# Optimization experiments

Measured on AMD Instinct MI355X. Metric: run time of the kernel, lower is better.

## Reference

```python
import jax, jax.numpy as jnp
import numpy as np

B, DIM, HEADS = 8, 1024, 8
DH = DIM // HEADS            # 128 = dim_head
MFEAT = 621                  # int(DH * log(DH)) performer features
MAXD = 4                     # max_rel_dist
IMG = 10                     # image side; source hardcodes stride 10 in scatter indices
L = IMG * IMG + 1            # geometry forces L = img_dim**2 + 1


def _geometry():
    m, K = MAXD, 2 * MAXD - 1
    base = np.arange(-m + 1, m)
    dx = np.broadcast_to(np.tile(base, K), (L, K * K))
    dy = np.broadcast_to(np.repeat(base, K), (L, K * K))
    x_off = np.concatenate([np.tile(np.arange(IMG), IMG), [0]])[:, None]
    y_off = np.concatenate([np.repeat(np.arange(IMG), IMG), [IMG]])[:, None]
    x_pos, y_pos = dx + x_off, dy + y_off
    diffs = np.abs(dx) + np.abs(dy)
    valid = (x_pos >= 0) & (x_pos < IMG) & (y_pos >= 0) & (y_pos < IMG) & (diffs < m)
    diffs = np.where(valid, diffs, m)  # invalid taps point at the max-dist encoding
    rel_window = (m - 1) * IMG + (m - 1)
    # scatter positions inside the unfold window (stride 10 hardcoded in source)
    indices = np.tile(np.arange(K), K) + np.repeat(np.arange(K) * 10, K)
    return jnp.asarray(diffs), jnp.asarray(valid), jnp.asarray(indices - rel_window)

DIFFS, VALID, OFFSETS = _geometry()  # [L,K2] int, [L,K2] bool, [K2] int


def softmax_kernel(data, proj, is_query, eps=1e-4):
    dn = data.shape[-1] ** -0.25
    ratio = proj.shape[0] ** -0.5
    dd = jnp.einsum('...id,jd->...ij', data * dn, proj)
    diag = (jnp.sum(data ** 2, -1) * (0.5 * dn * dn))[..., None]
    mx = jnp.max(dd, -1, keepdims=True) if is_query else jnp.max(dd)
    return ratio * (jnp.exp(dd - diag - mx) + eps)


def relative_attention(q, rpe, v):
    # q: [b,h,L,MFEAT] kernel features, rpe: [R,MFEAT], v: [b,h,L,DH]
    mde = rpe[-1]                                   # max-distance encoding
    v_sum = v.sum(-2)                               # [b,h,DH]
    q_dot = jnp.einsum('bhlm,rm->bhlr', q, rpe - mde)
    q_rel = jnp.take_along_axis(q_dot, DIFFS[None, None], axis=-1)  # [b,h,L,K2]
    q_rel = jnp.where(VALID[None, None], q_rel, 0.0)
    # gather v at relative offsets (equivalent to the zero-padded unfold +
    # sparse scatter of q_rel in the source, without the dense 67-wide window)
    pos = jnp.arange(L)[:, None] + OFFSETS[None, :]  # [L,K2]
    inb = (pos >= 0) & (pos < L)
    v_g = v[:, :, jnp.clip(pos, 0, L - 1), :]        # [b,h,L,K2,DH]
    v_g = jnp.where(inb[None, None, :, :, None], v_g, 0.0)
    denom = (rpe[DIFFS] - mde).sum(1) + mde * L      # [L,MFEAT]
    D_inv = 1.0 / jnp.einsum('bhlm,lm->bhl', q, denom)
    q_md = jnp.einsum('bhlm,m->bhl', q, mde)
    out = jnp.einsum('bhl,bhd->bhld', q_md, v_sum) + jnp.einsum('bhlk,bhlkd->bhld', q_rel, v_g)
    return out * D_inv[..., None]


def setup_inputs() -> dict:
    key = jax.random.key(0)
    ks = jax.random.split(key, 9)
    s = DIM ** -0.5
    return {
        'x': jax.random.normal(ks[0], (B, L, DIM), jnp.float32),
        'Wq': jax.random.normal(ks[1], (DIM, DIM), jnp.float32) * s,
        'bq': jnp.zeros((DIM,), jnp.float32),
        'Wv': jax.random.normal(ks[2], (DIM, DIM), jnp.float32) * s,
        'bv': jnp.zeros((DIM,), jnp.float32),
        'rpe': jax.random.normal(ks[3], (MAXD + 1, DH), jnp.float32) * 0.02,
        'proj': jax.random.normal(ks[4], (MFEAT, DH), jnp.float32),
        'Wo': jax.random.normal(ks[5], (DIM, DIM), jnp.float32) * s,
        'bo': jnp.zeros((DIM,), jnp.float32),
    }


def reference(x, Wq, bq, Wv, bv, rpe, proj, Wo, bo):
    b = x.shape[0]
    q = (x @ Wq.T + bq).reshape(b, L, HEADS, DH).transpose(0, 2, 1, 3)
    v = (x @ Wv.T + bv).reshape(b, L, HEADS, DH).transpose(0, 2, 1, 3)
    qf = softmax_kernel(q, proj, is_query=True)
    rf = softmax_kernel(rpe[None, None], proj, is_query=False)[0, 0]
    out = relative_attention(qf, rf, v)          # [b,h,L,DH]
    out = out.transpose(0, 2, 1, 3).reshape(b, L, DIM)
    return out @ Wo.T + bo
```

## Files before the change

kernel.cpp:

```cpp
#include <hip/hip_runtime.h>
#include <math.h>

namespace {

typedef __bf16 bf16_t;
typedef bf16_t bf16x8 __attribute__((ext_vector_type(8)));
typedef bf16_t bf16x4 __attribute__((ext_vector_type(4)));
typedef float f32x4 __attribute__((ext_vector_type(4)));

constexpr int B = 8, L = 101, DIM = 1024, H = 8, DH = 128, MF = 621, MFP = 640;
constexpr int BL = B * L;
constexpr int BLP = 832;
constexpr int BH = B * H;
constexpr int RR = BL * H;

constexpr float DN    = 0.29730177875068026f;
constexpr float DN2   = 0.08838834764831845f;
constexpr float RATIO = 0.04012861672f;
constexpr float EPS   = 1e-4f;

constexpr int NX = BL * DIM / 4;
constexpr int NP = MFP * 32;
constexpr int NR = 64 * DH / 4;
constexpr int NW = DIM * DIM / 4;
constexpr int NZ = 4 * (BLP - BL) * DIM / 4;
constexpr int NTOT = NX + NP + NR + 3 * NW + NZ;

__device__ __forceinline__ f32x4 mfma16(bf16x8 a, bf16x8 b, f32x4 c) {
  return __builtin_amdgcn_mfma_f32_16x16x32_bf16(a, b, c, 0, 0, 0);
}

__device__ __forceinline__ void split2(float f, bf16_t& h, bf16_t& l) {
  h = (bf16_t)f;
  l = (bf16_t)(f - (float)h);
}

__device__ __forceinline__ void gload_lds16(const bf16_t* g, bf16_t* l) {
  __builtin_amdgcn_global_load_lds(
      (const __attribute__((address_space(1))) void*)g,
      (__attribute__((address_space(3))) void*)l, 16, 0, 0);
}

__global__ __launch_bounds__(256) void split_all(const float* __restrict__ x,
                                                 const float* __restrict__ proj,
                                                 const float* __restrict__ rpe,
                                                 const float* __restrict__ Wq,
                                                 const float* __restrict__ Wv,
                                                 const float* __restrict__ Wo,
                                                 bf16_t* __restrict__ xh, bf16_t* __restrict__ xl,
                                                 bf16_t* __restrict__ ph,
                                                 bf16_t* __restrict__ rh, bf16_t* __restrict__ rl,
                                                 bf16_t* __restrict__ Wh,
                                                 bf16_t* __restrict__ Woh,
                                                 bf16_t* __restrict__ qh, bf16_t* __restrict__ ql) {
  const int u = blockIdx.x * 256 + threadIdx.x;
  if (u >= NTOT) return;
  auto emit2 = [](const float* s4, float sc, bf16_t* dh, bf16_t* dl, size_t off) {
    float4 f = *(const float4*)s4;
    bf16x4 hv, lv; bf16_t h, l;
    split2(f.x * sc, h, l); hv[0] = h; lv[0] = l;
    split2(f.y * sc, h, l); hv[1] = h; lv[1] = l;
    split2(f.z * sc, h, l); hv[2] = h; lv[2] = l;
    split2(f.w * sc, h, l); hv[3] = h; lv[3] = l;
    *(bf16x4*)(dh + off) = hv;
    *(bf16x4*)(dl + off) = lv;
  };
  auto emit1 = [](const float* s4, float sc, bf16_t* dh, size_t off) {
    float4 f = *(const float4*)s4;
    bf16x4 hv;
    hv[0] = (bf16_t)(f.x * sc); hv[1] = (bf16_t)(f.y * sc);
    hv[2] = (bf16_t)(f.z * sc); hv[3] = (bf16_t)(f.w * sc);
    *(bf16x4*)(dh + off) = hv;
  };
  int t = u;
  if (t < NX) { emit2(x + (size_t)t * 4, 1.f, xh, xl, (size_t)t * 4); return; }
  t -= NX;
  if (t < NP) {
    if ((t >> 5) < MF) emit1(proj + (size_t)t * 4, DN, ph, (size_t)t * 4);
    else { bf16x4 z = {}; *(bf16x4*)(ph + (size_t)t * 4) = z; }
    return;
  }
  t -= NP;
  if (t < NR) {
    if (t < 5 * DH / 4) emit2(rpe + (size_t)t * 4, 1.f, rh, rl, (size_t)t * 4);
    else { bf16x4 z = {}; *(bf16x4*)(rh + (size_t)t * 4) = z; *(bf16x4*)(rl + (size_t)t * 4) = z; }
    return;
  }
  t -= NR;
  if (t < NW) { emit1(Wq + (size_t)t * 4, 1.f, Wh, (size_t)t * 4); return; }
  t -= NW;
  if (t < NW) { emit1(Wv + (size_t)t * 4, 1.f, Wh, (size_t)(t + NW) * 4); return; }
  t -= NW;
  if (t < NW) { emit1(Wo + (size_t)t * 4, 1.f, Woh, (size_t)t * 4); return; }
  t -= NW;
  {
    const int buf = t / 6144, o = t % 6144;
    bf16_t* dst = (buf == 0) ? xh : (buf == 1) ? xl : (buf == 2) ? qh : ql;
    bf16x4 z = {};
    *(bf16x4*)(dst + (size_t)BL * DIM + (size_t)o * 4) = z;
  }
}

template<int MODE>
__global__ __launch_bounds__(256) void gemm64(const bf16_t* __restrict__ Ah,
                                              const bf16_t* __restrict__ Al,
                                              const bf16_t* __restrict__ Bh,
                                              const float* __restrict__ bias0,
                                              const float* __restrict__ bias1,
                                              float* __restrict__ Cf,
                                              bf16_t* __restrict__ Ch,
                                              bf16_t* __restrict__ Cl) {
  constexpr int K = 1024, BK = 64, NK = K / BK;
  __shared__ bf16_t lds[2][3][64 * 64];
  const int tid = threadIdx.x;
  const int w = tid >> 6, lane = tid & 63;
  const int wr = w >> 1, wc = w & 1;
  const int l15 = lane & 15, l4 = lane >> 4;
  const int rowBase = blockIdx.y * 64, colBase = blockIdx.x * 64;
  const int r8 = lane >> 3;
  const int cs = (lane & 7) ^ r8;
  const bf16_t* src = (w == 0) ? Ah : (w == 1) ? Al : Bh;
  const int grow0 = (w < 2) ? rowBase : colBase + ((w == 3) ? 32 : 0);
  const bf16_t* srcL = src + (size_t)(grow0 + r8) * K + cs * 8;
  const int tt = (w < 2) ? w : 2;
  const int dst0 = (w == 3) ? 32 * 64 : 0;
  auto STAGE = [&](int bf, int k0) {
    if (w < 2) {
#pragma unroll
      for (int j = 0; j < 8; ++j)
        gload_lds16(srcL + (size_t)(8 * j) * K + k0, &lds[bf][tt][j * 512]);
    } else {
#pragma unroll
      for (int j = 0; j < 4; ++j)
        gload_lds16(srcL + (size_t)(8 * j) * K + k0, &lds[bf][2][dst0 + j * 512]);
    }
  };
  const int ra0 = wr * 32 + l15, ra1 = ra0 + 16;
  const int rb0 = wc * 32 + l15, rb1 = rb0 + 16;
  auto TADDR = [](int row, int kg) { return row * 64 + (((kg) ^ (row & 7)) << 3); };
  f32x4 acc[2][2] = {};
  STAGE(0, 0);
  __syncthreads();
  int bf = 0;
  for (int ks = 0; ks < NK; ++ks) {
    if (ks + 1 < NK) STAGE(bf ^ 1, (ks + 1) * BK);
#pragma unroll
    for (int subk = 0; subk < 2; ++subk) {
      const int kg = subk * 4 + l4;
      bf16x8 a0h = *(const bf16x8*)&lds[bf][0][TADDR(ra0, kg)];
      bf16x8 a0l = *(const bf16x8*)&lds[bf][1][TADDR(ra0, kg)];
      bf16x8 a1h = *(const bf16x8*)&lds[bf][0][TADDR(ra1, kg)];
      bf16x8 a1l = *(const bf16x8*)&lds[bf][1][TADDR(ra1, kg)];
      bf16x8 b0  = *(const bf16x8*)&lds[bf][2][TADDR(rb0, kg)];
      bf16x8 b1  = *(const bf16x8*)&lds[bf][2][TADDR(rb1, kg)];
      acc[0][0] = mfma16(a0h, b0, acc[0][0]);
      acc[0][0] = mfma16(a0l, b0, acc[0][0]);
      acc[0][1] = mfma16(a0h, b1, acc[0][1]);
      acc[0][1] = mfma16(a0l, b1, acc[0][1]);
      acc[1][0] = mfma16(a1h, b0, acc[1][0]);
      acc[1][0] = mfma16(a1l, b0, acc[1][0]);
      acc[1][1] = mfma16(a1h, b1, acc[1][1]);
      acc[1][1] = mfma16(a1l, b1, acc[1][1]);
    }
    __syncthreads();
    bf ^= 1;
  }
#pragma unroll
  for (int ni = 0; ni < 2; ++ni) {
    const int col = colBase + wc * 32 + ni * 16 + l15;
#pragma unroll
    for (int mi = 0; mi < 2; ++mi) {
#pragma unroll
      for (int r2 = 0; r2 < 4; ++r2) {
        const int row = rowBase + wr * 32 + mi * 16 + l4 * 4 + r2;
        if (row < BL) {
          if (MODE == 0) {
            Cf[(size_t)row * 1024 + col] = acc[mi][ni][r2] + bias0[col];
          } else {
            if (col < 1024) {
              float val = acc[mi][ni][r2] + bias0[col];
              bf16_t h, lo; split2(val, h, lo);
              Ch[(size_t)row * 1024 + col] = h;
              Cl[(size_t)row * 1024 + col] = lo;
            } else {
              Cf[(size_t)row * 1024 + (col - 1024)] = acc[mi][ni][r2] + bias1[col - 1024];
            }
          }
        }
      }
    }
  }
}

__global__ __launch_bounds__(256) void qf3_kernel(const bf16_t* __restrict__ qh,
                                                  const bf16_t* __restrict__ ql,
                                                  const bf16_t* __restrict__ rh,
                                                  const bf16_t* __restrict__ rl,
                                                  const bf16_t* __restrict__ ph,
                                                  const float* __restrict__ rpe,
                                                  const float* __restrict__ v,
                                                  float* __restrict__ vsum,
                                                  float* __restrict__ fd) {
  const int tid = threadIdx.x;
  if (blockIdx.x >= 202) {
    const int bi = blockIdx.x - 202;
    const int half = tid >> 7, d = tid & 127;
    const int bh = bi * 2 + half;
    const int b = bh >> 3, h = bh & 7;
    const float* base = v + (size_t)(b * L) * DIM + h * DH + d;
    float s0 = 0.f, s1 = 0.f, s2 = 0.f, s3 = 0.f;
    int l = 0;
    for (; l + 4 <= L; l += 4) {
      s0 += base[(size_t)l * DIM];
      s1 += base[(size_t)(l + 1) * DIM];
      s2 += base[(size_t)(l + 2) * DIM];
      s3 += base[(size_t)(l + 3) * DIM];
    }
    for (; l < L; ++l) s0 += base[(size_t)l * DIM];
    vsum[(size_t)bh * DH + d] = s0 + s1 + s2 + s3;
    return;
  }
  __shared__ bf16_t Ahl[2][64 * 128];
  __shared__ bf16_t Bch[2][64 * 128];
  __shared__ float rfs[5][MFP];
  __shared__ float diag[32];
  __shared__ float diag5v[8];
  __shared__ float mxs[4][32];
  __shared__ float mxAll[32];
  __shared__ float mxrf[4];
  __shared__ float sred[4][32][5];
  const int w = tid >> 6, lane = tid & 63;
  const int l15 = lane & 15, l4 = lane >> 4;
  const int r0 = blockIdx.x * 32;
  const int r4 = lane >> 4;
  const int cg = lane & 15;
  {
    const bf16_t* srcA = (w == 0) ? qh : (w == 1) ? ql : (w == 2) ? rh : rl;
    const int arow0 = (w < 2) ? r0 : 0;
    bf16_t* dstA = &Ahl[w & 1][(w >= 2 ? 32 : 0) * 128];
    const bf16_t* peA = srcA + (size_t)(arow0 + r4) * DH + ((cg ^ r4) << 3);
    const bf16_t* poA = srcA + (size_t)(arow0 + r4) * DH + ((cg ^ r4 ^ 4) << 3);
#pragma unroll
    for (int j = 0; j < 8; ++j)
      gload_lds16(((j & 1) ? poA : peA) + (size_t)(4 * j) * DH, dstA + j * 512);
  }
  const bf16_t* peB = ph + (size_t)(w * 16 + r4) * DH + ((cg ^ r4) << 3);
  const bf16_t* poB = ph + (size_t)(w * 16 + r4) * DH + ((cg ^ r4 ^ 4) << 3);
  auto STAGE_B = [&](int buf, int c) {
    const size_t coff = (size_t)c * 64 * DH;
#pragma unroll
    for (int j = 0; j < 4; ++j)
      gload_lds16(((j & 1) ? poB : peB) + coff + (size_t)(4 * j) * DH,
                  &Bch[buf][(w * 16 + j * 4) * 128]);
  };
  {
    const int row = tid >> 3, ch = tid & 7;
    const size_t base = (size_t)(r0 + row) * DH + ch * 16;
    float s = 0.f;
#pragma unroll
    for (int t = 0; t < 2; ++t) {
      bf16x8 vh = *(const bf16x8*)(qh + base + t * 8);
      bf16x8 vl = *(const bf16x8*)(ql + base + t * 8);
#pragma unroll
      for (int e = 0; e < 8; ++e) {
        float f = (float)vh[e] + (float)vl[e];
        s += f * f;
      }
    }
    s += __shfl_xor(s, 1, 64); s += __shfl_xor(s, 2, 64); s += __shfl_xor(s, 4, 64);
    if (ch == 0) diag[row] = (0.5f * DN2) * s;
  }
  if (tid < 40) {
    const int row = tid >> 3, ch = tid & 7;
    float s = 0.f;
#pragma unroll
    for (int e = 0; e < 16; ++e) { float f = rpe[row * DH + ch * 16 + e]; s += f * f; }
    s += __shfl_xor(s, 1, 64); s += __shfl_xor(s, 2, 64); s += __shfl_xor(s, 4, 64);
    if (ch == 0) diag5v[row] = (0.5f * DN2) * s;
  }
  auto TADDR = [](int row, int kg) { return row * 128 + (((kg) ^ (row & 7)) << 3); };
  f32x4 acc[2][10] = {};
  f32x4 accr[10] = {};
  STAGE_B(0, 0);
  __syncthreads();
  int buf = 0;
#pragma unroll
  for (int c = 0; c < 10; ++c) {
    if (c + 1 < 10) STAGE_B(buf ^ 1, c + 1);
#pragma unroll
    for (int ks = 0; ks < 4; ++ks) {
      const int kg = ks * 4 + l4;
      bf16x8 a0h = *(const bf16x8*)&Ahl[0][TADDR(l15, kg)];
      bf16x8 a0l = *(const bf16x8*)&Ahl[1][TADDR(l15, kg)];
      bf16x8 a1h = *(const bf16x8*)&Ahl[0][TADDR(16 + l15, kg)];
      bf16x8 a1l = *(const bf16x8*)&Ahl[1][TADDR(16 + l15, kg)];
      bf16x8 arh = *(const bf16x8*)&Ahl[0][TADDR(32 + l15, kg)];
      bf16x8 arl = *(const bf16x8*)&Ahl[1][TADDR(32 + l15, kg)];
      bf16x8 bb  = *(const bf16x8*)&Bch[buf][TADDR(w * 16 + l15, kg)];
      acc[0][c] = mfma16(a0h, bb, acc[0][c]);
      acc[0][c] = mfma16(a0l, bb, acc[0][c]);
      acc[1][c] = mfma16(a1h, bb, acc[1][c]);
      acc[1][c] = mfma16(a1l, bb, acc[1][c]);
      accr[c]   = mfma16(arh, bb, accr[c]);
      accr[c]   = mfma16(arl, bb, accr[c]);
    }
    __syncthreads();
    buf ^= 1;
  }
  float pm[2][4];
#pragma unroll
  for (int mi = 0; mi < 2; ++mi)
#pragma unroll
    for (int r2 = 0; r2 < 4; ++r2) {
      float m = -3.4e38f;
#pragma unroll
      for (int ni = 0; ni < 10; ++ni) {
        const int col = ni * 64 + w * 16 + l15;
        float vv = (col < MF) ? acc[mi][ni][r2] : -3.4e38f;
        m = fmaxf(m, vv);
      }
      pm[mi][r2] = m;
    }
#pragma unroll
  for (int mask = 1; mask <= 8; mask <<= 1)
#pragma unroll
    for (int mi = 0; mi < 2; ++mi)
#pragma unroll
      for (int r2 = 0; r2 < 4; ++r2)
        pm[mi][r2] = fmaxf(pm[mi][r2], __shfl_xor(pm[mi][r2], mask, 64));
  if (l15 == 0) {
#pragma unroll
    for (int mi = 0; mi < 2; ++mi)
#pragma unroll
      for (int r2 = 0; r2 < 4; ++r2)
        mxs[w][mi * 16 + l4 * 4 + r2] = pm[mi][r2];
  }
  {
    float m = -3.4e38f;
#pragma unroll
    for (int ni = 0; ni < 10; ++ni) {
      const int col = ni * 64 + w * 16 + l15;
#pragma unroll
      for (int r2 = 0; r2 < 4; ++r2) {
        const int row5 = l4 * 4 + r2;
        if (row5 < 5 && col < MF) m = fmaxf(m, accr[ni][r2]);
      }
    }
#pragma unroll
    for (int mask = 1; mask <= 32; mask <<= 1) m = fmaxf(m, __shfl_xor(m, mask, 64));
    if (lane == 0) mxrf[w] = m;
  }
  __syncthreads();
  {
    const float mxR = fmaxf(fmaxf(mxrf[0], mxrf[1]), fmaxf(mxrf[2], mxrf[3]));
#pragma unroll
    for (int ni = 0; ni < 10; ++ni) {
      const int col = ni * 64 + w * 16 + l15;
#pragma unroll
      for (int r2 = 0; r2 < 4; ++r2) {
        const int row5 = l4 * 4 + r2;
        if (row5 < 5) {
          float val = (col < MF)
              ? RATIO * (__expf(accr[ni][r2] - diag5v[row5] - mxR) + EPS) : 0.f;
          rfs[row5][col] = val;
        }
      }
    }
  }
  if (tid < 32)
    mxAll[tid] = fmaxf(fmaxf(mxs[0][tid], mxs[1][tid]), fmaxf(mxs[2][tid], mxs[3][tid]));
  __syncthreads();
  for (int i = tid; i < 4 * MFP; i += 256) rfs[i / MFP][i % MFP] -= rfs[4][i % MFP];
  __syncthreads();
  float s[2][4][5] = {};
#pragma unroll
  for (int mi = 0; mi < 2; ++mi)
#pragma unroll
    for (int r2 = 0; r2 < 4; ++r2) {
      const int row = mi * 16 + l4 * 4 + r2;
      const float sub = diag[row] + mxAll[row];
#pragma unroll
      for (int ni = 0; ni < 10; ++ni) {
        const int col = ni * 64 + w * 16 + l15;
        const float qfv = RATIO * (__expf(acc[mi][ni][r2] - sub) + EPS);
#pragma unroll
        for (int c = 0; c < 5; ++c) s[mi][r2][c] += qfv * rfs[c][col];
      }
    }
#pragma unroll
  for (int mask = 1; mask <= 8; mask <<= 1)
#pragma unroll
    for (int mi = 0; mi < 2; ++mi)
#pragma unroll
      for (int r2 = 0; r2 < 4; ++r2)
#pragma unroll
        for (int c = 0; c < 5; ++c)
          s[mi][r2][c] += __shfl_xor(s[mi][r2][c], mask, 64);
  if (l15 == 0) {
#pragma unroll
    for (int mi = 0; mi < 2; ++mi)
#pragma unroll
      for (int r2 = 0; r2 < 4; ++r2)
#pragma unroll
        for (int c = 0; c < 5; ++c)
          sred[w][mi * 16 + l4 * 4 + r2][c] = s[mi][r2][c];
  }
  __syncthreads();
  if (tid < 160) {
    const int row = tid / 5, c = tid % 5;
    fd[(size_t)(r0 + row) * 8 + c] =
        sred[0][row][c] + sred[1][row][c] + sred[2][row][c] + sred[3][row][c];
  }
}

__global__ __launch_bounds__(256) void out_kernel(const float* __restrict__ fd,
                                                  const float* __restrict__ v,
                                                  const float* __restrict__ vsum,
                                                  bf16_t* __restrict__ attnh,
                                                  bf16_t* __restrict__ attnl) {
  const int tid = threadIdx.x;
  const int sub = tid >> 7, d = tid & 127;
  const int bh = blockIdx.y, b = bh >> 3, h = bh & 7;
  const int l = blockIdx.x * 2 + sub;
  if (l >= L) return;
  const size_t r = (size_t)(b * L + l) * H + h;
  const float q0 = fd[r * 8 + 0], q1 = fd[r * 8 + 1], q2 = fd[r * 8 + 2],
              q3 = fd[r * 8 + 3], sM = fd[r * 8 + 4];
  float o = sM * vsum[(size_t)bh * DH + d];
  float c0 = 0, c1 = 0, c2 = 0, c3 = 0;
  const int xo = (l < 100) ? (l % 10) : 0;
  const int yo = (l < 100) ? (l / 10) : 10;
#pragma unroll
  for (int k = 0; k < 49; ++k) {
    const int dx = (k % 7) - 3, dy = (k / 7) - 3;
    const int xp = xo + dx, yp = yo + dy;
    const int df = (dx < 0 ? -dx : dx) + (dy < 0 ? -dy : dy);
    if (xp >= 0 && xp < 10 && yp >= 0 && yp < 10 && df < 4) {
      float qq;
      if (df == 0)      { c0 += 1.f; qq = q0; }
      else if (df == 1) { c1 += 1.f; qq = q1; }
      else if (df == 2) { c2 += 1.f; qq = q2; }
      else              { c3 += 1.f; qq = q3; }
      const int pos = l + dx + 10 * dy;
      o += qq * v[(size_t)(b * L + pos) * DIM + h * DH + d];
    }
  }
  const float D = c0 * q0 + c1 * q1 + c2 * q2 + c3 * q3 + (float)L * sM;
  const float val = o / D;
  bf16_t hi, lo; split2(val, hi, lo);
  const size_t oi = (size_t)(b * L + l) * DIM + h * DH + d;
  attnh[oi] = hi;
  attnl[oi] = lo;
}

}

extern "C" void kernel_launch(void* const* d_in, const int* in_sizes, int n_in,
                              void* d_out, int out_size, void* d_ws, size_t ws_size,
                              hipStream_t stream) {
  const float* x    = (const float*)d_in[0];
  const float* Wq   = (const float*)d_in[1];
  const float* bq   = (const float*)d_in[2];
  const float* Wv   = (const float*)d_in[3];
  const float* bv   = (const float*)d_in[4];
  const float* rpe  = (const float*)d_in[5];
  const float* proj = (const float*)d_in[6];
  const float* Wo   = (const float*)d_in[7];
  const float* bo   = (const float*)d_in[8];

  char* p = (char*)d_ws;
  auto alloc = [&](size_t bytes) { char* r = p; p += (bytes + 255) & ~255ull; return r; };
  bf16_t* xh  = (bf16_t*)alloc((size_t)BLP * DIM * 2);
  bf16_t* xl  = (bf16_t*)alloc((size_t)BLP * DIM * 2);
  bf16_t* Wh  = (bf16_t*)alloc((size_t)2 * DIM * DIM * 2);
  bf16_t* Woh = (bf16_t*)alloc((size_t)DIM * DIM * 2);
  bf16_t* ph  = (bf16_t*)alloc((size_t)MFP * DH * 2);
  bf16_t* rh  = (bf16_t*)alloc((size_t)64 * DH * 2);
  bf16_t* rl  = (bf16_t*)alloc((size_t)64 * DH * 2);
  bf16_t* qh  = (bf16_t*)alloc((size_t)BLP * DIM * 2);
  bf16_t* ql  = (bf16_t*)alloc((size_t)BLP * DIM * 2);
  float*  v   = (float*)alloc((size_t)BL * DIM * 4);
  float*  fd  = (float*)alloc((size_t)RR * 8 * 4);
  float*  vsm = (float*)alloc((size_t)BH * DH * 4);

  split_all<<<(NTOT + 255) / 256, 256, 0, stream>>>(x, proj, rpe, Wq, Wv, Wo,
                                                    xh, xl, ph, rh, rl,
                                                    Wh, Woh, qh, ql);
  gemm64<1><<<dim3(32, 13), 256, 0, stream>>>(xh, xl, Wh, bq, bv, v, qh, ql);
  qf3_kernel<<<202 + 32, 256, 0, stream>>>(qh, ql, rh, rl, ph, rpe, v, vsm, fd);
  out_kernel<<<dim3((L + 1) / 2, BH), 256, 0, stream>>>(fd, v, vsm, qh, ql);
  gemm64<0><<<dim3(16, 13), 256, 0, stream>>>(qh, ql, Woh, bo, nullptr,
                                              (float*)d_out, nullptr, nullptr);
}
```

Measured before the change: 76.95 us.

## Fuse attention output into feature kernel and compute v-sum in GEMM epilogue

Result: slower. 138.1 us (+79.5%).

```diff
diff --git a/kernel.cpp b/kernel.cpp
--- a/kernel.cpp
+++ b/kernel.cpp
@@ -24,7 +24,8 @@
 constexpr int NR = 64 * DH / 4;
 constexpr int NW = DIM * DIM / 4;
 constexpr int NZ = 4 * (BLP - BL) * DIM / 4;
-constexpr int NTOT = NX + NP + NR + 3 * NW + NZ;
+constexpr int NV = BH * DH / 4;
+constexpr int NTOT = NX + NP + NR + 3 * NW + NZ + NV;
 
 __device__ __forceinline__ f32x4 mfma16(bf16x8 a, bf16x8 b, f32x4 c) {
   return __builtin_amdgcn_mfma_f32_16x16x32_bf16(a, b, c, 0, 0, 0);
@@ -52,7 +53,8 @@
                                                  bf16_t* __restrict__ rh, bf16_t* __restrict__ rl,
                                                  bf16_t* __restrict__ Wh,
                                                  bf16_t* __restrict__ Woh,
-                                                 bf16_t* __restrict__ qh, bf16_t* __restrict__ ql) {
+                                                 bf16_t* __restrict__ qh, bf16_t* __restrict__ ql,
+                                                 float* __restrict__ vsum) {
   const int u = blockIdx.x * 256 + threadIdx.x;
   if (u >= NTOT) return;
   auto emit2 = [](const float* s4, float sc, bf16_t* dh, bf16_t* dl, size_t off) {
@@ -93,12 +95,15 @@
   t -= NW;
   if (t < NW) { emit1(Wo + (size_t)t * 4, 1.f, Woh, (size_t)t * 4); return; }
   t -= NW;
-  {
+  if (t < NZ) {
     const int buf = t / 6144, o = t % 6144;
     bf16_t* dst = (buf == 0) ? xh : (buf == 1) ? xl : (buf == 2) ? qh : ql;
     bf16x4 z = {};
     *(bf16x4*)(dst + (size_t)BL * DIM + (size_t)o * 4) = z;
-  }
+    return;
+  }
+  t -= NZ;
+  ((float4*)vsum)[t] = make_float4(0.f, 0.f, 0.f, 0.f);
 }
 
 template<int MODE>
@@ -109,7 +114,8 @@
                                               const float* __restrict__ bias1,
                                               float* __restrict__ Cf,
                                               bf16_t* __restrict__ Ch,
-                                              bf16_t* __restrict__ Cl) {
+                                              bf16_t* __restrict__ Cl,
+                                              float* __restrict__ vsum) {
   constexpr int K = 1024, BK = 64, NK = K / BK;
   __shared__ bf16_t lds[2][3][64 * 64];
   const int tid = threadIdx.x;
@@ -170,6 +176,8 @@
     const int col = colBase + wc * 32 + ni * 16 + l15;
 #pragma unroll
     for (int mi = 0; mi < 2; ++mi) {
+      float vpart = 0.f;
+      int curb = -1;
 #pragma unroll
       for (int r2 = 0; r2 < 4; ++r2) {
         const int row = rowBase + wr * 32 + mi * 16 + l4 * 4 + r2;
@@ -183,11 +191,22 @@
               Ch[(size_t)row * 1024 + col] = h;
               Cl[(size_t)row * 1024 + col] = lo;
             } else {
-              Cf[(size_t)row * 1024 + (col - 1024)] = acc[mi][ni][r2] + bias1[col - 1024];
+              const int vcol = col - 1024;
+              const float val = acc[mi][ni][r2] + bias1[vcol];
+              Cf[(size_t)row * 1024 + vcol] = val;
+              const int b = row / L;
+              if (b != curb) {
+                if (curb >= 0)
+                  atomicAdd(&vsum[(size_t)(curb * 8) * DH + vcol], vpart);
+                curb = b; vpart = 0.f;
+              }
+              vpart += val;
             }
           }
         }
       }
+      if (MODE == 1 && curb >= 0)
+        atomicAdd(&vsum[(size_t)(curb * 8) * DH + (col - 1024)], vpart);
     }
   }
 }
@@ -199,27 +218,10 @@
                                                   const bf16_t* __restrict__ ph,
                                                   const float* __restrict__ rpe,
                                                   const float* __restrict__ v,
-                                                  float* __restrict__ vsum,
-                                                  float* __restrict__ fd) {
+                                                  const float* __restrict__ vsum,
+                                                  bf16_t* __restrict__ attnh,
+                                                  bf16_t* __restrict__ attnl) {
   const int tid = threadIdx.x;
-  if (blockIdx.x >= 202) {
-    const int bi = blockIdx.x - 202;
-    const int half = tid >> 7, d = tid & 127;
-    const int bh = bi * 2 + half;
-    const int b = bh >> 3, h = bh & 7;
-    const float* base = v + (size_t)(b * L) * DIM + h * DH + d;
-    float s0 = 0.f, s1 = 0.f, s2 = 0.f, s3 = 0.f;
-    int l = 0;
-    for (; l + 4 <= L; l += 4) {
-      s0 += base[(size_t)l * DIM];
-      s1 += base[(size_t)(l + 1) * DIM];
-      s2 += base[(size_t)(l + 2) * DIM];
-      s3 += base[(size_t)(l + 3) * DIM];
-    }
-    for (; l < L; ++l) s0 += base[(size_t)l * DIM];
-    vsum[(size_t)bh * DH + d] = s0 + s1 + s2 + s3;
-    return;
-  }
   __shared__ bf16_t Ahl[2][64 * 128];
   __shared__ bf16_t Bch[2][64 * 128];
   __shared__ float rfs[5][MFP];
@@ -229,6 +231,7 @@
   __shared__ float mxAll[32];
   __shared__ float mxrf[4];
   __shared__ float sred[4][32][5];
+  __shared__ float fdv[32][6];
   const int w = tid >> 6, lane = tid & 63;
   const int l15 = lane & 15, l4 = lane >> 4;
   const int r0 = blockIdx.x * 32;
@@ -408,49 +411,59 @@
   __syncthreads();
   if (tid < 160) {
     const int row = tid / 5, c = tid % 5;
-    fd[(size_t)(r0 + row) * 8 + c] =
-        sred[0][row][c] + sred[1][row][c] + sred[2][row][c] + sred[3][row][c];
-  }
-}
-
-__global__ __launch_bounds__(256) void out_kernel(const float* __restrict__ fd,
-                                                  const float* __restrict__ v,
-                                                  const float* __restrict__ vsum,
-                                                  bf16_t* __restrict__ attnh,
-                                                  bf16_t* __restrict__ attnl) {
-  const int tid = threadIdx.x;
-  const int sub = tid >> 7, d = tid & 127;
-  const int bh = blockIdx.y, b = bh >> 3, h = bh & 7;
-  const int l = blockIdx.x * 2 + sub;
-  if (l >= L) return;
-  const size_t r = (size_t)(b * L + l) * H + h;
-  const float q0 = fd[r * 8 + 0], q1 = fd[r * 8 + 1], q2 = fd[r * 8 + 2],
-              q3 = fd[r * 8 + 3], sM = fd[r * 8 + 4];
-  float o = sM * vsum[(size_t)bh * DH + d];
-  float c0 = 0, c1 = 0, c2 = 0, c3 = 0;
-  const int xo = (l < 100) ? (l % 10) : 0;
-  const int yo = (l < 100) ? (l / 10) : 10;
-#pragma unroll
-  for (int k = 0; k < 49; ++k) {
-    const int dx = (k % 7) - 3, dy = (k / 7) - 3;
-    const int xp = xo + dx, yp = yo + dy;
-    const int df = (dx < 0 ? -dx : dx) + (dy < 0 ? -dy : dy);
-    if (xp >= 0 && xp < 10 && yp >= 0 && yp < 10 && df < 4) {
-      float qq;
-      if (df == 0)      { c0 += 1.f; qq = q0; }
-      else if (df == 1) { c1 += 1.f; qq = q1; }
-      else if (df == 2) { c2 += 1.f; qq = q2; }
-      else              { c3 += 1.f; qq = q3; }
-      const int pos = l + dx + 10 * dy;
-      o += qq * v[(size_t)(b * L + pos) * DIM + h * DH + d];
-    }
-  }
-  const float D = c0 * q0 + c1 * q1 + c2 * q2 + c3 * q3 + (float)L * sM;
-  const float val = o / D;
-  bf16_t hi, lo; split2(val, hi, lo);
-  const size_t oi = (size_t)(b * L + l) * DIM + h * DH + d;
-  attnh[oi] = hi;
-  attnl[oi] = lo;
+    fdv[row][c] = sred[0][row][c] + sred[1][row][c] + sred[2][row][c] + sred[3][row][c];
+  }
+  __syncthreads();
+  if (tid < 32) {
+    const int blg = (r0 >> 3) + (tid >> 3);
+    const int l = blg % L;
+    const int xo = (l < 100) ? (l % 10) : 0;
+    const int yo = (l < 100) ? (l / 10) : 10;
+    float c0 = 0, c1 = 0, c2 = 0, c3 = 0;
+#pragma unroll
+    for (int k = 0; k < 49; ++k) {
+      const int dx = (k % 7) - 3, dy = (k / 7) - 3;
+      const int xp = xo + dx, yp = yo + dy;
+      const int df = (dx < 0 ? -dx : dx) + (dy < 0 ? -dy : dy);
+      if (xp >= 0 && xp < 10 && yp >= 0 && yp < 10 && df < 4) {
+        if (df == 0) c0 += 1.f; else if (df == 1) c1 += 1.f;
+        else if (df == 2) c2 += 1.f; else c3 += 1.f;
+      }
+    }
+    const float D = c0 * fdv[tid][0] + c1 * fdv[tid][1] + c2 * fdv[tid][2] +
+                    c3 * fdv[tid][3] + (float)L * fdv[tid][4];
+    fdv[tid][5] = 1.f / D;
+  }
+  __syncthreads();
+#pragma unroll
+  for (int bl = 0; bl < 4; ++bl) {
+    const int blg = (r0 >> 3) + bl;
+    const int b = blg / L, l = blg % L;
+    const int xo = (l < 100) ? (l % 10) : 0;
+    const int yo = (l < 100) ? (l / 10) : 10;
+#pragma unroll
+    for (int hh = 0; hh < 8; hh += 2) {
+      const int h = hh + (tid >> 7), d = tid & 127;
+      const int row = bl * 8 + h;
+      float o = fdv[row][4] * vsum[(size_t)(b * 8 + h) * DH + d];
+      const float* vb = v + (size_t)(b * L) * DIM + h * DH + d;
+#pragma unroll
+      for (int k = 0; k < 49; ++k) {
+        const int dx = (k % 7) - 3, dy = (k / 7) - 3;
+        const int xp = xo + dx, yp = yo + dy;
+        const int df = (dx < 0 ? -dx : dx) + (dy < 0 ? -dy : dy);
+        if (xp >= 0 && xp < 10 && yp >= 0 && yp < 10 && df < 4) {
+          const int pos = l + dx + 10 * dy;
+          o += fdv[row][df] * vb[(size_t)pos * DIM];
+        }
+      }
+      const float val = o * fdv[row][5];
+      bf16_t hi, lo; split2(val, hi, lo);
+      const size_t oi = (size_t)(b * L + l) * DIM + h * DH + d;
+      attnh[oi] = hi;
+      attnl[oi] = lo;
+    }
+  }
 }
 
 }
@@ -480,15 +493,13 @@
   bf16_t* qh  = (bf16_t*)alloc((size_t)BLP * DIM * 2);
   bf16_t* ql  = (bf16_t*)alloc((size_t)BLP * DIM * 2);
   float*  v   = (float*)alloc((size_t)BL * DIM * 4);
-  float*  fd  = (float*)alloc((size_t)RR * 8 * 4);
   float*  vsm = (float*)alloc((size_t)BH * DH * 4);
 
   split_all<<<(NTOT + 255) / 256, 256, 0, stream>>>(x, proj, rpe, Wq, Wv, Wo,
                                                     xh, xl, ph, rh, rl,
-                                                    Wh, Woh, qh, ql);
-  gemm64<1><<<dim3(32, 13), 256, 0, stream>>>(xh, xl, Wh, bq, bv, v, qh, ql);
-  qf3_kernel<<<202 + 32, 256, 0, stream>>>(qh, ql, rh, rl, ph, rpe, v, vsm, fd);
-  out_kernel<<<dim3((L + 1) / 2, BH), 256, 0, stream>>>(fd, v, vsm, qh, ql);
+                                                    Wh, Woh, qh, ql, vsm);
+  gemm64<1><<<dim3(32, 13), 256, 0, stream>>>(xh, xl, Wh, bq, bv, v, qh, ql, vsm);
+  qf3_kernel<<<202, 256, 0, stream>>>(qh, ql, rh, rl, ph, rpe, v, vsm, qh, ql);
   gemm64<0><<<dim3(16, 13), 256, 0, stream>>>(qh, ql, Woh, bo, nullptr,
-                                              (float*)d_out, nullptr, nullptr);
-}
+                                              (float*)d_out, nullptr, nullptr, nullptr);
+}
```

## Drop x low-bf16 split in QV GEMM and fuse v-sum into its epilogue

Applied to the files above, without the earlier changes.

Result: no change. 76.78 us (-0.2%).

```diff
diff --git a/kernel.cpp b/kernel.cpp
--- a/kernel.cpp
+++ b/kernel.cpp
@@ -23,8 +23,9 @@
 constexpr int NP = MFP * 32;
 constexpr int NR = 64 * DH / 4;
 constexpr int NW = DIM * DIM / 4;
-constexpr int NZ = 4 * (BLP - BL) * DIM / 4;
-constexpr int NTOT = NX + NP + NR + 3 * NW + NZ;
+constexpr int NZ = 3 * (BLP - BL) * DIM / 4;
+constexpr int NV = BH * DH / 4;
+constexpr int NTOT = NX + NP + NR + 3 * NW + NZ + NV;
 
 __device__ __forceinline__ f32x4 mfma16(bf16x8 a, bf16x8 b, f32x4 c) {
   return __builtin_amdgcn_mfma_f32_16x16x32_bf16(a, b, c, 0, 0, 0);
@@ -47,12 +48,13 @@
                                                  const float* __restrict__ Wq,
                                                  const float* __restrict__ Wv,
                                                  const float* __restrict__ Wo,
-                                                 bf16_t* __restrict__ xh, bf16_t* __restrict__ xl,
+                                                 bf16_t* __restrict__ xh,
                                                  bf16_t* __restrict__ ph,
                                                  bf16_t* __restrict__ rh, bf16_t* __restrict__ rl,
                                                  bf16_t* __restrict__ Wh,
                                                  bf16_t* __restrict__ Woh,
-                                                 bf16_t* __restrict__ qh, bf16_t* __restrict__ ql) {
+                                                 bf16_t* __restrict__ qh, bf16_t* __restrict__ ql,
+                                                 float* __restrict__ vsum) {
   const int u = blockIdx.x * 256 + threadIdx.x;
   if (u >= NTOT) return;
   auto emit2 = [](const float* s4, float sc, bf16_t* dh, bf16_t* dl, size_t off) {
@@ -73,7 +75,7 @@
     *(bf16x4*)(dh + off) = hv;
   };
   int t = u;
-  if (t < NX) { emit2(x + (size_t)t * 4, 1.f, xh, xl, (size_t)t * 4); return; }
+  if (t < NX) { emit1(x + (size_t)t * 4, 1.f, xh, (size_t)t * 4); return; }
   t -= NX;
   if (t < NP) {
     if ((t >> 5) < MF) emit1(proj + (size_t)t * 4, DN, ph, (size_t)t * 4);
@@ -93,15 +95,18 @@
   t -= NW;
   if (t < NW) { emit1(Wo + (size_t)t * 4, 1.f, Woh, (size_t)t * 4); return; }
   t -= NW;
-  {
+  if (t < NZ) {
     const int buf = t / 6144, o = t % 6144;
-    bf16_t* dst = (buf == 0) ? xh : (buf == 1) ? xl : (buf == 2) ? qh : ql;
+    bf16_t* dst = (buf == 0) ? xh : (buf == 1) ? qh : ql;
     bf16x4 z = {};
     *(bf16x4*)(dst + (size_t)BL * DIM + (size_t)o * 4) = z;
-  }
-}
-
-template<int MODE>
+    return;
+  }
+  t -= NZ;
+  ((float4*)vsum)[t] = make_float4(0.f, 0.f, 0.f, 0.f);
+}
+
+template<int MODE, int AT>
 __global__ __launch_bounds__(256) void gemm64(const bf16_t* __restrict__ Ah,
                                               const bf16_t* __restrict__ Al,
                                               const bf16_t* __restrict__ Bh,
@@ -109,9 +114,11 @@
                                               const float* __restrict__ bias1,
                                               float* __restrict__ Cf,
                                               bf16_t* __restrict__ Ch,
-                                              bf16_t* __restrict__ Cl) {
+                                              bf16_t* __restrict__ Cl,
+                                              float* __restrict__ vsum) {
   constexpr int K = 1024, BK = 64, NK = K / BK;
-  __shared__ bf16_t lds[2][3][64 * 64];
+  constexpr int NT = AT + 1;
+  __shared__ bf16_t lds[2][NT][64 * 64];
   const int tid = threadIdx.x;
   const int w = tid >> 6, lane = tid & 63;
   const int wr = w >> 1, wc = w & 1;
@@ -119,24 +126,34 @@
   const int rowBase = blockIdx.y * 64, colBase = blockIdx.x * 64;
   const int r8 = lane >> 3;
   const int cs = (lane & 7) ^ r8;
-  const bf16_t* src = (w == 0) ? Ah : (w == 1) ? Al : Bh;
-  const int grow0 = (w < 2) ? rowBase : colBase + ((w == 3) ? 32 : 0);
+  const bf16_t* src;
+  int grow0, ti, dst0;
+  if (AT == 2) {
+    src = (w == 0) ? Ah : (w == 1) ? Al : Bh;
+    grow0 = (w < 2) ? rowBase : colBase + ((w == 3) ? 32 : 0);
+    ti = (w < 2) ? w : 2;
+    dst0 = (w == 3) ? 32 * 64 : 0;
+  } else {
+    src = (w < 2) ? Ah : Bh;
+    grow0 = ((w < 2) ? rowBase : colBase) + ((w & 1) ? 32 : 0);
+    ti = (w < 2) ? 0 : 1;
+    dst0 = (w & 1) ? 32 * 64 : 0;
+  }
   const bf16_t* srcL = src + (size_t)(grow0 + r8) * K + cs * 8;
-  const int tt = (w < 2) ? w : 2;
-  const int dst0 = (w == 3) ? 32 * 64 : 0;
   auto STAGE = [&](int bf, int k0) {
-    if (w < 2) {
+    if (AT == 2 && w < 2) {
 #pragma unroll
       for (int j = 0; j < 8; ++j)
-        gload_lds16(srcL + (size_t)(8 * j) * K + k0, &lds[bf][tt][j * 512]);
+        gload_lds16(srcL + (size_t)(8 * j) * K + k0, &lds[bf][ti][j * 512]);
     } else {
 #pragma unroll
       for (int j = 0; j < 4; ++j)
-        gload_lds16(srcL + (size_t)(8 * j) * K + k0, &lds[bf][2][dst0 + j * 512]);
+        gload_lds16(srcL + (size_t)(8 * j) * K + k0, &lds[bf][ti][dst0 + j * 512]);
     }
   };
   const int ra0 = wr * 32 + l15, ra1 = ra0 + 16;
   const int rb0 = wc * 32 + l15, rb1 = rb0 + 16;
+  constexpr int bt = (AT == 1) ? 1 : 2;
   auto TADDR = [](int row, int kg) { return row * 64 + (((kg) ^ (row & 7)) << 3); };
   f32x4 acc[2][2] = {};
   STAGE(0, 0);
@@ -148,19 +165,21 @@
     for (int subk = 0; subk < 2; ++subk) {
       const int kg = subk * 4 + l4;
       bf16x8 a0h = *(const bf16x8*)&lds[bf][0][TADDR(ra0, kg)];
-      bf16x8 a0l = *(const bf16x8*)&lds[bf][1][TADDR(ra0, kg)];
       bf16x8 a1h = *(const bf16x8*)&lds[bf][0][TADDR(ra1, kg)];
-      bf16x8 a1l = *(const bf16x8*)&lds[bf][1][TADDR(ra1, kg)];
-      bf16x8 b0  = *(const bf16x8*)&lds[bf][2][TADDR(rb0, kg)];
-      bf16x8 b1  = *(const bf16x8*)&lds[bf][2][TADDR(rb1, kg)];
+      bf16x8 b0  = *(const bf16x8*)&lds[bf][bt][TADDR(rb0, kg)];
+      bf16x8 b1  = *(const bf16x8*)&lds[bf][bt][TADDR(rb1, kg)];
       acc[0][0] = mfma16(a0h, b0, acc[0][0]);
-      acc[0][0] = mfma16(a0l, b0, acc[0][0]);
       acc[0][1] = mfma16(a0h, b1, acc[0][1]);
-      acc[0][1] = mfma16(a0l, b1, acc[0][1]);
       acc[1][0] = mfma16(a1h, b0, acc[1][0]);
-      acc[1][0] = mfma16(a1l, b0, acc[1][0]);
       acc[1][1] = mfma16(a1h, b1, acc[1][1]);
-      acc[1][1] = mfma16(a1l, b1, acc[1][1]);
+      if (AT == 2) {
+        bf16x8 a0l = *(const bf16x8*)&lds[bf][1][TADDR(ra0, kg)];
+        bf16x8 a1l = *(const bf16x8*)&lds[bf][1][TADDR(ra1, kg)];
+        acc[0][0] = mfma16(a0l, b0, acc[0][0]);
+        acc[0][1] = mfma16(a0l, b1, acc[0][1]);
+        acc[1][0] = mfma16(a1l, b0, acc[1][0]);
+        acc[1][1] = mfma16(a1l, b1, acc[1][1]);
+      }
     }
     __syncthreads();
     bf ^= 1;
@@ -170,6 +189,8 @@
     const int col = colBase + wc * 32 + ni * 16 + l15;
 #pragma unroll
     for (int mi = 0; mi < 2; ++mi) {
+      float vpart = 0.f;
+      int curb = -1;
 #pragma unroll
       for (int r2 = 0; r2 < 4; ++r2) {
         const int row = rowBase + wr * 32 + mi * 16 + l4 * 4 + r2;
@@ -183,11 +204,22 @@
               Ch[(size_t)row * 1024 + col] = h;
               Cl[(size_t)row * 1024 + col] = lo;
             } else {
-              Cf[(size_t)row * 1024 + (col - 1024)] = acc[mi][ni][r2] + bias1[col - 1024];
+              const int vcol = col - 1024;
+              const float val = acc[mi][ni][r2] + bias1[vcol];
+              Cf[(size_t)row * 1024 + vcol] = val;
+              const int b = row / L;
+              if (b != curb) {
+                if (curb >= 0)
+                  atomicAdd(&vsum[(size_t)(curb * 8) * DH + vcol], vpart);
+                curb = b; vpart = 0.f;
+              }
+              vpart += val;
             }
           }
         }
       }
+      if (MODE == 1 && curb >= 0)
+        atomicAdd(&vsum[(size_t)(curb * 8) * DH + (col - 1024)], vpart);
     }
   }
 }
@@ -198,28 +230,8 @@
                                                   const bf16_t* __restrict__ rl,
                                                   const bf16_t* __restrict__ ph,
                                                   const float* __restrict__ rpe,
-                                                  const float* __restrict__ v,
-                                                  float* __restrict__ vsum,
                                                   float* __restrict__ fd) {
   const int tid = threadIdx.x;
-  if (blockIdx.x >= 202) {
-    const int bi = blockIdx.x - 202;
-    const int half = tid >> 7, d = tid & 127;
-    const int bh = bi * 2 + half;
-    const int b = bh >> 3, h = bh & 7;
-    const float* base = v + (size_t)(b * L) * DIM + h * DH + d;
-    float s0 = 0.f, s1 = 0.f, s2 = 0.f, s3 = 0.f;
-    int l = 0;
-    for (; l + 4 <= L; l += 4) {
-      s0 += base[(size_t)l * DIM];
-      s1 += base[(size_t)(l + 1) * DIM];
-      s2 += base[(size_t)(l + 2) * DIM];
-      s3 += base[(size_t)(l + 3) * DIM];
-    }
-    for (; l < L; ++l) s0 += base[(size_t)l * DIM];
-    vsum[(size_t)bh * DH + d] = s0 + s1 + s2 + s3;
-    return;
-  }
   __shared__ bf16_t Ahl[2][64 * 128];
   __shared__ bf16_t Bch[2][64 * 128];
   __shared__ float rfs[5][MFP];
@@ -471,7 +483,6 @@
   char* p = (char*)d_ws;
   auto alloc = [&](size_t bytes) { char* r = p; p += (bytes + 255) & ~255ull; return r; };
   bf16_t* xh  = (bf16_t*)alloc((size_t)BLP * DIM * 2);
-  bf16_t* xl  = (bf16_t*)alloc((size_t)BLP * DIM * 2);
   bf16_t* Wh  = (bf16_t*)alloc((size_t)2 * DIM * DIM * 2);
   bf16_t* Woh = (bf16_t*)alloc((size_t)DIM * DIM * 2);
   bf16_t* ph  = (bf16_t*)alloc((size_t)MFP * DH * 2);
@@ -484,11 +495,12 @@
   float*  vsm = (float*)alloc((size_t)BH * DH * 4);
 
   split_all<<<(NTOT + 255) / 256, 256, 0, stream>>>(x, proj, rpe, Wq, Wv, Wo,
-                                                    xh, xl, ph, rh, rl,
-                                                    Wh, Woh, qh, ql);
-  gemm64<1><<<dim3(32, 13), 256, 0, stream>>>(xh, xl, Wh, bq, bv, v, qh, ql);
-  qf3_kernel<<<202 + 32, 256, 0, stream>>>(qh, ql, rh, rl, ph, rpe, v, vsm, fd);
+                                                    xh, ph, rh, rl,
+                                                    Wh, Woh, qh, ql, vsm);
+  gemm64<1, 1><<<dim3(32, 13), 256, 0, stream>>>(xh, nullptr, Wh, bq, bv,
+                                                 v, qh, ql, vsm);
+  qf3_kernel<<<202, 256, 0, stream>>>(qh, ql, rh, rl, ph, rpe, fd);
   out_kernel<<<dim3((L + 1) / 2, BH), 256, 0, stream>>>(fd, v, vsm, qh, ql);
-  gemm64<0><<<dim3(16, 13), 256, 0, stream>>>(qh, ql, Woh, bo, nullptr,
-                                              (float*)d_out, nullptr, nullptr);
-}
+  gemm64<0, 2><<<dim3(16, 13), 256, 0, stream>>>(qh, ql, Woh, bo, nullptr,
+                                                 (float*)d_out, nullptr, nullptr, nullptr);
+}
```
